# Kernel optimization log

Measured on AMD Instinct MI355X. Metric: run time of the kernel, lower is better.

The kernel has to match this reference:

```python
import jax, jax.numpy as jnp
import numpy as np

B, S, D, H = 4, 2048, 2048, 16
HD = D // H  # 128
ROPE_THETA = 10000.0


def apply_rope(x, pos, theta=ROPE_THETA):
    # x: [b, h, s, d], pos: [s] int. Interleaved-pair RoPE.
    d = x.shape[-1]
    inv_freq = theta ** (-jnp.arange(0, d, 2, dtype=jnp.float32) / d)  # [d/2]
    ang = pos.astype(jnp.float32)[:, None] * inv_freq[None, :]         # [s, d/2]
    cos, sin = jnp.cos(ang), jnp.sin(ang)
    x1, x2 = x[..., ::2], x[..., 1::2]                                  # [b,h,s,d/2]
    r1 = x1 * cos - x2 * sin
    r2 = x1 * sin + x2 * cos
    return jnp.stack([r1, r2], axis=-1).reshape(x.shape).astype(x.dtype)


def setup_inputs() -> dict:
    key = jax.random.key(0)
    kx, kq, kk, kv, ko = jax.random.split(key, 5)
    w_scale = 0.02
    return {
        "x": jax.random.normal(kx, (B, S, D), dtype=jnp.float32),
        "wq": jax.random.normal(kq, (D, D), dtype=jnp.float32) * w_scale,
        "wk": jax.random.normal(kk, (D, D), dtype=jnp.float32) * w_scale,
        "wv": jax.random.normal(kv, (D, D), dtype=jnp.float32) * w_scale,
        "wo": jax.random.normal(ko, (D, D), dtype=jnp.float32) * w_scale,
        "token_positions": jnp.arange(S, dtype=jnp.int32),
    }


def reference(x, wq, wk, wv, wo, token_positions):
    b, s, d = x.shape
    # QKV projections: weight layout is [d_out, d_in] (torch nn.Parameter convention)
    Q = jnp.einsum("bsd,kd->bsk", x, wq).reshape(b, s, H, HD).transpose(0, 2, 1, 3)
    K = jnp.einsum("bsd,kd->bsk", x, wk).reshape(b, s, H, HD).transpose(0, 2, 1, 3)
    V = jnp.einsum("bsd,kd->bsk", x, wv).reshape(b, s, H, HD).transpose(0, 2, 1, 3)
    Q = apply_rope(Q, token_positions)
    K = apply_rope(K, token_positions)
    # naive causal attention: full [b,h,s,s] score matrix
    scores = jnp.einsum("bhqd,bhkd->bhqk", Q, K) / jnp.sqrt(jnp.float32(HD))
    causal = jnp.tril(jnp.ones((s, s), dtype=bool))
    neg_inf = jnp.finfo(scores.dtype).min
    scores = jnp.where(causal[None, None], scores, neg_inf)
    probs = jax.nn.softmax(scores, axis=-1)
    O = jnp.einsum("bhqk,bhkd->bhqd", probs, V)
    O = O.transpose(0, 2, 1, 3).reshape(b, s, H * HD)
    return jnp.einsum("bsv,dv->bsd", O, wo)
```

## Files before the change

### kernel.cpp

```cpp
#include <hip/hip_runtime.h>
#include <cstdint>

typedef _Float16 f16;
typedef __attribute__((ext_vector_type(8))) _Float16 f16x8;
typedef __attribute__((ext_vector_type(4))) float f32x4;

constexpr int Bc  = 4;
constexpr int Sc  = 2048;
constexpr int Dc  = 2048;
constexpr int Hc  = 16;
constexpr int HDc = 128;
constexpr int LDq = 3 * Dc;

__global__ void cast_all_kernel(const float* __restrict__ x,  const float* __restrict__ wq,
                                const float* __restrict__ wk, const float* __restrict__ wv,
                                const float* __restrict__ wo,
                                f16* __restrict__ xh,  f16* __restrict__ wqh,
                                f16* __restrict__ wkh, f16* __restrict__ wvh,
                                f16* __restrict__ woh)
{
    long bid = blockIdx.x;
    const float* src; f16* dst; long off;
    if (bid < 8192)       { src = x;  dst = xh;  off = bid * 2048; }
    else {
        int r = (int)((bid - 8192) >> 11);
        off = ((bid - 8192) & 2047) * 2048;
        switch (r) {
            case 0:  src = wq; dst = wqh; break;
            case 1:  src = wk; dst = wkh; break;
            case 2:  src = wv; dst = wvh; break;
            default: src = wo; dst = woh; break;
        }
    }
    long i = off + (long)threadIdx.x * 8;
    float4 a = *(const float4*)(src + i);
    float4 b = *(const float4*)(src + i + 4);
    f16x8 o = { (f16)a.x, (f16)a.y, (f16)a.z, (f16)a.w,
                (f16)b.x, (f16)b.y, (f16)b.z, (f16)b.w };
    *(f16x8*)(dst + i) = o;
}

__global__ void gen_rope_tab(const int* __restrict__ pos, float2* __restrict__ tab)
{
    int s = blockIdx.x, i = threadIdx.x;
    float inv = expf(-(float)i * (9.210340371976184f / 64.0f));
    float ang = (float)pos[s] * inv;
    float sn, cs;
    sincosf(ang, &sn, &cs);
    tab[s * 64 + i] = make_float2(cs, sn);
}

__device__ __forceinline__ void async_cp16(const f16* g, f16* l)
{
    __builtin_amdgcn_global_load_lds(
        (__attribute__((address_space(1))) void*)(g),
        (__attribute__((address_space(3))) void*)(l), 16, 0, 0);
}

template<typename OUT_T, bool ROPE>
__global__ __launch_bounds__(512, 2) void gemm_bt8(
    const f16* __restrict__ A, const f16* __restrict__ W,
    OUT_T* __restrict__ C, const float2* __restrict__ tab,
    int M, int N, int K)
{
    __shared__ alignas(16) f16 As[4][8192];
    __shared__ alignas(16) f16 Bs[4][8192];

    const int tid  = threadIdx.x;
    const int wave = tid >> 6, lane = tid & 63;
    const int l16  = lane & 15, quad = lane >> 4;
    const int wm   = wave >> 2, wn = wave & 3;

    const int nwg = (int)gridDim.x;
    int bid = (int)blockIdx.x;
    int wg  = ((nwg & 7) == 0) ? ((bid & 7) * (nwg >> 3) + (bid >> 3)) : bid;
    const int ntile = N >> 8;
    const int mt = wg / ntile, nt = wg % ntile;
    const int m0 = mt << 8, n0 = nt << 8;

    const int  prow = tid >> 2;
    const int  lch  = (((tid & 3) ^ ((prow >> 1) & 3)) << 3);
    const f16* Asrc = A + (long)(m0 + prow) * K + lch;
    const f16* Bsrc = W + (long)(n0 + prow) * K + lch;
    const long rsk  = (long)K << 7;
    const int  dst0 = wave << 9;

    const int nkt = K >> 5;

    auto stA = [&](int kt) {
        const f16* g = Asrc + ((long)kt << 5);
        int s = kt & 3;
        async_cp16(g,       &As[s][dst0]);
        async_cp16(g + rsk, &As[s][4096 + dst0]);
    };
    auto stB = [&](int kt) {
        const f16* g = Bsrc + ((long)kt << 5);
        int s = kt & 3;
        async_cp16(g,       &Bs[s][dst0]);
        async_cp16(g + rsk, &Bs[s][4096 + dst0]);
    };

    const int coff = ((quad ^ ((l16 >> 1) & 3)) << 3);
    const int arow = wm * 128 + l16;
    const int brow = wn * 64  + l16;

    f32x4 acc[8][4];
#pragma unroll
    for (int i = 0; i < 8; i++)
#pragma unroll
        for (int j = 0; j < 4; j++) acc[i][j] = (f32x4){0.f, 0.f, 0.f, 0.f};

    stA(0); stB(0);
    if (nkt > 1) {
        stA(1); stB(1);
        asm volatile("s_waitcnt vmcnt(4)" ::: "memory");
    } else {
        asm volatile("s_waitcnt vmcnt(0)" ::: "memory");
    }
    __builtin_amdgcn_s_barrier();
    __builtin_amdgcn_sched_barrier(0);

    for (int kt = 0; kt < nkt; ++kt) {
        const int s = kt & 3;
        const f16* as = &As[s][(long)arow * 32 + coff];
        const f16* bs = &Bs[s][(long)brow * 32 + coff];

        f16x8 bfr[4], afr[4];
#pragma unroll
        for (int j = 0; j < 4; ++j) bfr[j] = *(const f16x8*)(bs + j * 512);
#pragma unroll
        for (int i = 0; i < 4; ++i) afr[i] = *(const f16x8*)(as + i * 512);
        if (kt + 2 < nkt) stA(kt + 2);
        asm volatile("s_waitcnt lgkmcnt(0)" ::: "memory");
        __builtin_amdgcn_sched_barrier(0);
        __builtin_amdgcn_s_setprio(1);
#pragma unroll
        for (int i = 0; i < 4; ++i)
#pragma unroll
            for (int j = 0; j < 4; ++j)
                acc[i][j] = __builtin_amdgcn_mfma_f32_16x16x32_f16(afr[i], bfr[j], acc[i][j], 0, 0, 0);
        __builtin_amdgcn_s_setprio(0);

        f16x8 afr2[4];
#pragma unroll
        for (int i = 0; i < 4; ++i) afr2[i] = *(const f16x8*)(as + (i + 4) * 512);
        if (kt + 2 < nkt) stB(kt + 2);
        asm volatile("s_waitcnt lgkmcnt(0)" ::: "memory");
        __builtin_amdgcn_sched_barrier(0);
        __builtin_amdgcn_s_setprio(1);
#pragma unroll
        for (int i = 0; i < 4; ++i)
#pragma unroll
            for (int j = 0; j < 4; ++j)
                acc[i + 4][j] = __builtin_amdgcn_mfma_f32_16x16x32_f16(afr2[i], bfr[j], acc[i + 4][j], 0, 0, 0);
        __builtin_amdgcn_s_setprio(0);

        if (kt + 2 < nkt) asm volatile("s_waitcnt vmcnt(4)" ::: "memory");
        else              asm volatile("s_waitcnt vmcnt(0)" ::: "memory");
        __builtin_amdgcn_s_barrier();
        __builtin_amdgcn_sched_barrier(0);
    }

#pragma unroll
    for (int i = 0; i < 8; ++i) {
        int row = m0 + wm * 128 + i * 16 + quad * 4;
#pragma unroll
        for (int j = 0; j < 4; ++j) {
            int col = n0 + wn * 64 + j * 16 + l16;
            if (ROPE && col < 4096) {
                const int  ip = (col & 127) >> 1;
                const bool ev = !(col & 1);
#pragma unroll
                for (int r = 0; r < 4; ++r) {
                    float v = acc[i][j][r];
                    float p = __shfl_xor(v, 1, 64);
                    int   sfx = (row + r) & (Sc - 1);
                    float2 cs = tab[sfx * 64 + ip];
                    float o = ev ? (v * cs.x - p * cs.y) : (p * cs.y + v * cs.x);
                    C[(long)(row + r) * N + col] = (OUT_T)o;
                }
            } else {
#pragma unroll
                for (int r = 0; r < 4; ++r)
                    C[(long)(row + r) * N + col] = (OUT_T)acc[i][j][r];
            }
        }
    }
}

__device__ __forceinline__ int swz(int row, int col, int ldshift) {
    return (row << ldshift) + (((((col >> 3) ^ ((row >> 1) & 7)) << 3) | (col & 7)));
}

__global__ __launch_bounds__(256, 2) void attn_kernel(
    const f16* __restrict__ Q, const f16* __restrict__ Kg,
    const f16* __restrict__ Vg, f16* __restrict__ O)
{
    __shared__ alignas(16) f16 Kt[64 * 128];
    __shared__ alignas(16) f16 Vt[128 * 64];
    __shared__ alignas(16) f16 Pl[128 * 64];

    const int tid  = threadIdx.x;
    const int wave = tid >> 6, lane = tid & 63;
    const int l16  = lane & 15, quad = lane >> 4;

    const int L  = (int)blockIdx.x;
    const int bh = (L & 7) + 8 * (L >> 7);
    const int qi = 15 - ((L >> 3) & 15);
    const int b  = bh >> 4, h = bh & 15;
    const long bi = (long)b * Sc * LDq + (long)h * HDc;
    const long bo = (long)b * Sc * Dc  + (long)h * HDc;
    const float cexp = 0.12751742366f;

    long koff[4];
    f16* kdst[4];
#pragma unroll
    for (int j = 0; j < 4; j++) {
        int row_l = j * 16 + wave * 4 + (lane >> 4);
        int chg   = (lane & 15) ^ ((row_l >> 1) & 7);
        koff[j]   = bi + (long)row_l * LDq + chg * 8;
        kdst[j]   = (f16*)&Kt[(j * 16 + wave * 4) * 128];
    }
    const int vd0 = lane * 2;

    f16x8 ones;
#pragma unroll
    for (int i = 0; i < 8; i++) ones[i] = (f16)1.0f;

    unsigned int vreg[2][8];
    auto load_v = [&](int k0) {
#pragma unroll
        for (int j = 0; j < 2; j++) {
            int kk0 = wave * 8 + j * 32;
#pragma unroll
            for (int i2 = 0; i2 < 8; i2++)
                vreg[j][i2] = *(const unsigned int*)&Vg[bi + (long)(k0 + kk0 + i2) * LDq + vd0];
        }
    };
    auto load_k_async = [&](int k0) {
#pragma unroll
        for (int j = 0; j < 4; j++)
            async_cp16(Kg + koff[j] + (long)k0 * LDq, kdst[j]);
    };

    const int q0  = qi * 128;
    const int nkt = 2 * qi + 2;
    const int rlo = q0 + wave * 32;

    f16x8 qf[2][4];
#pragma unroll
    for (int im = 0; im < 2; im++)
#pragma unroll
        for (int kk = 0; kk < 4; kk++)
            qf[im][kk] = *(const f16x8*)&Q[bi + (long)(q0 + wave * 32 + im * 16 + l16) * LDq
                                           + kk * 32 + quad * 8];

    f32x4 oacc[2][8];
    f32x4 lacc[2];
#pragma unroll
    for (int im = 0; im < 2; im++) {
        lacc[im] = (f32x4){0.f, 0.f, 0.f, 0.f};
#pragma unroll
        for (int nt = 0; nt < 8; nt++) oacc[im][nt] = (f32x4){0.f, 0.f, 0.f, 0.f};
    }

    load_k_async(0);
    load_v(0);
    for (int kt = 0; kt < nkt; kt++) {
        const int k0 = kt * 64;
        __syncthreads();
#pragma unroll
        for (int j = 0; j < 2; j++) {
            int kk0 = wave * 8 + j * 32;
            f16x8 lo, hi;
#pragma unroll
            for (int i2 = 0; i2 < 8; i2++) {
                lo[i2] = ((const f16*)&vreg[j][i2])[0];
                hi[i2] = ((const f16*)&vreg[j][i2])[1];
            }
            *(f16x8*)&Vt[swz(vd0,     kk0, 6)] = lo;
            *(f16x8*)&Vt[swz(vd0 + 1, kk0, 6)] = hi;
        }
        __syncthreads();

        const bool compute = (k0 <= rlo + 31);
        if (compute) {
            f32x4 sf[2][4];
#pragma unroll
            for (int im = 0; im < 2; im++)
#pragma unroll
                for (int in = 0; in < 4; in++) sf[im][in] = (f32x4){0.f, 0.f, 0.f, 0.f};
#pragma unroll
            for (int kk = 0; kk < 4; kk++) {
                f16x8 bf[4];
#pragma unroll
                for (int in = 0; in < 4; in++)
                    bf[in] = *(const f16x8*)&Kt[swz(in * 16 + l16, kk * 32 + quad * 8, 7)];
#pragma unroll
                for (int im = 0; im < 2; im++)
#pragma unroll
                    for (int in = 0; in < 4; in++)
                        sf[im][in] = __builtin_amdgcn_mfma_f32_16x16x32_f16(qf[im][kk], bf[in], sf[im][in], 0, 0, 0);
            }

#pragma unroll
            for (int im = 0; im < 2; im++) {
                const int rbase = rlo + im * 16;
                const bool need_mask = (k0 + 63 > rbase);
#pragma unroll
                for (int in = 0; in < 4; in++) {
#pragma unroll
                    for (int r = 0; r < 4; r++) {
                        float p = __builtin_amdgcn_exp2f(sf[im][in][r] * cexp);
                        if (need_mask) {
                            int kc  = k0 + in * 16 + l16;
                            int row = rbase + quad * 4 + r;
                            p = (kc <= row) ? p : 0.f;
                        }
                        Pl[swz(wave * 32 + im * 16 + quad * 4 + r, in * 16 + l16, 6)] = (f16)p;
                    }
                }
            }
        }
        __syncthreads();

        if (kt + 1 < nkt) {
            load_k_async(k0 + 64);
            load_v(k0 + 64);
        }

        if (compute) {
#pragma unroll
            for (int kk = 0; kk < 2; kk++) {
                f16x8 pf[2];
#pragma unroll
                for (int im = 0; im < 2; im++)
                    pf[im] = *(const f16x8*)&Pl[swz(wave * 32 + im * 16 + l16, kk * 32 + quad * 8, 6)];
#pragma unroll
                for (int im = 0; im < 2; im++)
                    lacc[im] = __builtin_amdgcn_mfma_f32_16x16x32_f16(pf[im], ones, lacc[im], 0, 0, 0);
#pragma unroll
                for (int nt = 0; nt < 8; nt++) {
                    f16x8 vf = *(const f16x8*)&Vt[swz(nt * 16 + l16, kk * 32 + quad * 8, 6)];
#pragma unroll
                    for (int im = 0; im < 2; im++)
                        oacc[im][nt] = __builtin_amdgcn_mfma_f32_16x16x32_f16(pf[im], vf, oacc[im][nt], 0, 0, 0);
                }
            }
        }
    }

#pragma unroll
    for (int im = 0; im < 2; im++) {
        int qrow = q0 + wave * 32 + im * 16 + quad * 4;
#pragma unroll
        for (int r = 0; r < 4; r++) {
            float inv = 1.0f / lacc[im][r];
#pragma unroll
            for (int nt = 0; nt < 8; nt++)
                O[bo + (long)(qrow + r) * Dc + nt * 16 + l16] = (f16)(oacc[im][nt][r] * inv);
        }
    }
}

extern "C" void kernel_launch(void* const* d_in, const int* in_sizes, int n_in,
                              void* d_out, int out_size, void* d_ws, size_t ws_size,
                              hipStream_t stream)
{
    const float* x  = (const float*)d_in[0];
    const float* wq = (const float*)d_in[1];
    const float* wk = (const float*)d_in[2];
    const float* wv = (const float*)d_in[3];
    const float* wo = (const float*)d_in[4];
    const int*  pos = (const int*)d_in[5];
    float* out = (float*)d_out;

    const long E  = (long)Bc * Sc * Dc;
    const long W  = (long)Dc * Dc;
    const long EQ = (long)Bc * Sc * LDq;
    f16* ws   = (f16*)d_ws;
    f16* xh   = ws;
    f16* wqh  = ws + E;
    f16* wkh  = wqh + W;
    f16* wvh  = wkh + W;
    f16* woh  = wvh + W;
    f16* QKV  = woh + W;
    float2* tab = (float2*)(QKV + EQ);
    f16* Oh   = xh;

    cast_all_kernel<<<dim3(16384), 256, 0, stream>>>(x, wq, wk, wv, wo,
                                                     xh, wqh, wkh, wvh, woh);
    gen_rope_tab<<<dim3(Sc), 64, 0, stream>>>(pos, tab);

    dim3 gq((Bc * Sc / 256) * (3 * Dc / 256));
    gemm_bt8<f16, true><<<gq, 512, 0, stream>>>(xh, wqh, QKV, tab,
                                                Bc * Sc, 3 * Dc, Dc);

    attn_kernel<<<dim3(1024), 256, 0, stream>>>(QKV, QKV + Dc, QKV + 2 * Dc, Oh);

    dim3 gg((Bc * Sc / 256) * (Dc / 256));
    gemm_bt8<float, false><<<gg, 512, 0, stream>>>(Oh, woh, out, nullptr,
                                                   Bc * Sc, Dc, Dc);
}
```

Measured before the change: 618.2 us.

## Deepen GEMM prefetch to three stages and split QKV into separate buffers

```diff
diff --git a/kernel.cpp b/kernel.cpp
--- a/kernel.cpp
+++ b/kernel.cpp
@@ -10,7 +10,7 @@
 constexpr int Dc  = 2048;
 constexpr int Hc  = 16;
 constexpr int HDc = 128;
-constexpr int LDq = 3 * Dc;
+constexpr long Ec = (long)Bc * Sc * Dc;
 
 __global__ void cast_all_kernel(const float* __restrict__ x,  const float* __restrict__ wq,
                                 const float* __restrict__ wk, const float* __restrict__ wv,
@@ -111,12 +111,11 @@
         for (int j = 0; j < 4; j++) acc[i][j] = (f32x4){0.f, 0.f, 0.f, 0.f};
 
     stA(0); stB(0);
-    if (nkt > 1) {
-        stA(1); stB(1);
-        asm volatile("s_waitcnt vmcnt(4)" ::: "memory");
-    } else {
-        asm volatile("s_waitcnt vmcnt(0)" ::: "memory");
-    }
+    if (nkt > 1) { stA(1); stB(1); }
+    if (nkt > 2) { stA(2); stB(2); }
+    if (nkt > 2)      asm volatile("s_waitcnt vmcnt(8)" ::: "memory");
+    else if (nkt > 1) asm volatile("s_waitcnt vmcnt(4)" ::: "memory");
+    else              asm volatile("s_waitcnt vmcnt(0)" ::: "memory");
     __builtin_amdgcn_s_barrier();
     __builtin_amdgcn_sched_barrier(0);
 
@@ -130,7 +129,7 @@
         for (int j = 0; j < 4; ++j) bfr[j] = *(const f16x8*)(bs + j * 512);
 #pragma unroll
         for (int i = 0; i < 4; ++i) afr[i] = *(const f16x8*)(as + i * 512);
-        if (kt + 2 < nkt) stA(kt + 2);
+        if (kt + 3 < nkt) stA(kt + 3);
         asm volatile("s_waitcnt lgkmcnt(0)" ::: "memory");
         __builtin_amdgcn_sched_barrier(0);
         __builtin_amdgcn_s_setprio(1);
@@ -144,7 +143,7 @@
         f16x8 afr2[4];
 #pragma unroll
         for (int i = 0; i < 4; ++i) afr2[i] = *(const f16x8*)(as + (i + 4) * 512);
-        if (kt + 2 < nkt) stB(kt + 2);
+        if (kt + 3 < nkt) stB(kt + 3);
         asm volatile("s_waitcnt lgkmcnt(0)" ::: "memory");
         __builtin_amdgcn_sched_barrier(0);
         __builtin_amdgcn_s_setprio(1);
@@ -155,8 +154,9 @@
                 acc[i + 4][j] = __builtin_amdgcn_mfma_f32_16x16x32_f16(afr2[i], bfr[j], acc[i + 4][j], 0, 0, 0);
         __builtin_amdgcn_s_setprio(0);
 
-        if (kt + 2 < nkt) asm volatile("s_waitcnt vmcnt(4)" ::: "memory");
-        else              asm volatile("s_waitcnt vmcnt(0)" ::: "memory");
+        if (kt + 3 < nkt)      asm volatile("s_waitcnt vmcnt(8)" ::: "memory");
+        else if (kt + 2 < nkt) asm volatile("s_waitcnt vmcnt(4)" ::: "memory");
+        else if (kt + 1 < nkt) asm volatile("s_waitcnt vmcnt(0)" ::: "memory");
         __builtin_amdgcn_s_barrier();
         __builtin_amdgcn_sched_barrier(0);
     }
@@ -167,17 +167,26 @@
 #pragma unroll
         for (int j = 0; j < 4; ++j) {
             int col = n0 + wn * 64 + j * 16 + l16;
-            if (ROPE && col < 4096) {
-                const int  ip = (col & 127) >> 1;
-                const bool ev = !(col & 1);
-#pragma unroll
-                for (int r = 0; r < 4; ++r) {
-                    float v = acc[i][j][r];
-                    float p = __shfl_xor(v, 1, 64);
-                    int   sfx = (row + r) & (Sc - 1);
-                    float2 cs = tab[sfx * 64 + ip];
-                    float o = ev ? (v * cs.x - p * cs.y) : (p * cs.y + v * cs.x);
-                    C[(long)(row + r) * N + col] = (OUT_T)o;
+            if (ROPE) {
+                const int  reg  = col >> 11;
+                const int  coll = col & 2047;
+                OUT_T* Co = C + (long)reg * Ec;
+                if (reg < 2) {
+                    const int  ip = (coll & 127) >> 1;
+                    const bool ev = !(coll & 1);
+#pragma unroll
+                    for (int r = 0; r < 4; ++r) {
+                        float v = acc[i][j][r];
+                        float p = __shfl_xor(v, 1, 64);
+                        int   sfx = (row + r) & (Sc - 1);
+                        float2 cs = tab[sfx * 64 + ip];
+                        float o = ev ? (v * cs.x - p * cs.y) : (p * cs.y + v * cs.x);
+                        Co[(long)(row + r) * 2048 + coll] = (OUT_T)o;
+                    }
+                } else {
+#pragma unroll
+                    for (int r = 0; r < 4; ++r)
+                        Co[(long)(row + r) * 2048 + coll] = (OUT_T)acc[i][j][r];
                 }
             } else {
 #pragma unroll
@@ -208,8 +217,7 @@
     const int bh = (L & 7) + 8 * (L >> 7);
     const int qi = 15 - ((L >> 3) & 15);
     const int b  = bh >> 4, h = bh & 15;
-    const long bi = (long)b * Sc * LDq + (long)h * HDc;
-    const long bo = (long)b * Sc * Dc  + (long)h * HDc;
+    const long base = (long)b * Sc * Dc + (long)h * HDc;
     const float cexp = 0.12751742366f;
 
     long koff[4];
@@ -218,7 +226,7 @@
     for (int j = 0; j < 4; j++) {
         int row_l = j * 16 + wave * 4 + (lane >> 4);
         int chg   = (lane & 15) ^ ((row_l >> 1) & 7);
-        koff[j]   = bi + (long)row_l * LDq + chg * 8;
+        koff[j]   = base + (long)row_l * Dc + chg * 8;
         kdst[j]   = (f16*)&Kt[(j * 16 + wave * 4) * 128];
     }
     const int vd0 = lane * 2;
@@ -234,13 +242,13 @@
             int kk0 = wave * 8 + j * 32;
 #pragma unroll
             for (int i2 = 0; i2 < 8; i2++)
-                vreg[j][i2] = *(const unsigned int*)&Vg[bi + (long)(k0 + kk0 + i2) * LDq + vd0];
+                vreg[j][i2] = *(const unsigned int*)&Vg[base + (long)(k0 + kk0 + i2) * Dc + vd0];
         }
     };
     auto load_k_async = [&](int k0) {
 #pragma unroll
         for (int j = 0; j < 4; j++)
-            async_cp16(Kg + koff[j] + (long)k0 * LDq, kdst[j]);
+            async_cp16(Kg + koff[j] + (long)k0 * Dc, kdst[j]);
     };
 
     const int q0  = qi * 128;
@@ -252,7 +260,7 @@
     for (int im = 0; im < 2; im++)
 #pragma unroll
         for (int kk = 0; kk < 4; kk++)
-            qf[im][kk] = *(const f16x8*)&Q[bi + (long)(q0 + wave * 32 + im * 16 + l16) * LDq
+            qf[im][kk] = *(const f16x8*)&Q[base + (long)(q0 + wave * 32 + im * 16 + l16) * Dc
                                            + kk * 32 + quad * 8];
 
     f32x4 oacc[2][8];
@@ -358,7 +366,7 @@
             float inv = 1.0f / lacc[im][r];
 #pragma unroll
             for (int nt = 0; nt < 8; nt++)
-                O[bo + (long)(qrow + r) * Dc + nt * 16 + l16] = (f16)(oacc[im][nt][r] * inv);
+                O[base + (long)(qrow + r) * Dc + nt * 16 + l16] = (f16)(oacc[im][nt][r] * inv);
         }
     }
 }
@@ -375,17 +383,17 @@
     const int*  pos = (const int*)d_in[5];
     float* out = (float*)d_out;
 
-    const long E  = (long)Bc * Sc * Dc;
     const long W  = (long)Dc * Dc;
-    const long EQ = (long)Bc * Sc * LDq;
     f16* ws   = (f16*)d_ws;
     f16* xh   = ws;
-    f16* wqh  = ws + E;
+    f16* wqh  = ws + Ec;
     f16* wkh  = wqh + W;
     f16* wvh  = wkh + W;
     f16* woh  = wvh + W;
-    f16* QKV  = woh + W;
-    float2* tab = (float2*)(QKV + EQ);
+    f16* Qh   = woh + W;
+    f16* Kh   = Qh + Ec;
+    f16* Vh   = Kh + Ec;
+    float2* tab = (float2*)(Vh + Ec);
     f16* Oh   = xh;
 
     cast_all_kernel<<<dim3(16384), 256, 0, stream>>>(x, wq, wk, wv, wo,
@@ -393,10 +401,10 @@
     gen_rope_tab<<<dim3(Sc), 64, 0, stream>>>(pos, tab);
 
     dim3 gq((Bc * Sc / 256) * (3 * Dc / 256));
-    gemm_bt8<f16, true><<<gq, 512, 0, stream>>>(xh, wqh, QKV, tab,
+    gemm_bt8<f16, true><<<gq, 512, 0, stream>>>(xh, wqh, Qh, tab,
                                                 Bc * Sc, 3 * Dc, Dc);
 
-    attn_kernel<<<dim3(1024), 256, 0, stream>>>(QKV, QKV + Dc, QKV + 2 * Dc, Oh);
+    attn_kernel<<<dim3(1024), 256, 0, stream>>>(Qh, Kh, Vh, Oh);
 
     dim3 gg((Bc * Sc / 256) * (Dc / 256));
     gemm_bt8<float, false><<<gg, 512, 0, stream>>>(Oh, woh, out, nullptr,
```

Result: no change. 612.3 us (-1.0%).
